# Kernel tuning notes

Hardware: AMD Instinct MI355X
Metric: run time of the kernel (lower is better)

The kernel has to match this reference:

```python
import jax, jax.numpy as jnp
import numpy as np

N_NODES = 100000
N_EDGES = 3200000
N_GRAPHS = 2048
MOL_DIM = 78
HID = 32
OUT = 128
N_LAYERS = 5
BN_EPS = 1e-5


def setup_inputs() -> dict:
    key = jax.random.key(0)
    ks = jax.random.split(key, 16)
    x = jax.random.normal(ks[0], (N_NODES, MOL_DIM), dtype=jnp.float32)
    edge_index = jax.random.randint(ks[1], (2, N_EDGES), 0, N_NODES, dtype=jnp.int32)
    batch = jnp.sort(jax.random.randint(ks[2], (N_NODES,), 0, N_GRAPHS, dtype=jnp.int32))
    def lin(k, fan_in, shape):
        b = 1.0 / np.sqrt(fan_in)
        return jax.random.uniform(k, shape, jnp.float32, -b, b)
    # layer 0 MLP (78 -> 32 -> 32)
    w1_0 = lin(ks[3], MOL_DIM, (MOL_DIM, HID))
    b1_0 = lin(ks[4], MOL_DIM, (HID,))
    w2_0 = lin(ks[5], HID, (HID, HID))
    b2_0 = lin(ks[6], HID, (HID,))
    # layers 1..4 MLPs (32 -> 32 -> 32), stacked
    w1 = lin(ks[7], HID, (N_LAYERS - 1, HID, HID))
    b1 = lin(ks[8], HID, (N_LAYERS - 1, HID))
    w2 = lin(ks[9], HID, (N_LAYERS - 1, HID, HID))
    b2 = lin(ks[10], HID, (N_LAYERS - 1, HID))
    # BatchNorm affine params per layer
    gamma = jnp.ones((N_LAYERS, HID), jnp.float32)
    beta = jnp.zeros((N_LAYERS, HID), jnp.float32)
    # final fc (32 -> 128)
    fc_w = lin(ks[11], HID, (HID, OUT))
    fc_b = lin(ks[12], HID, (OUT,))
    return {"x": x, "edge_index": edge_index, "batch": batch,
            "w1_0": w1_0, "b1_0": b1_0, "w2_0": w2_0, "b2_0": b2_0,
            "w1": w1, "b1": b1, "w2": w2, "b2": b2,
            "gamma": gamma, "beta": beta, "fc_w": fc_w, "fc_b": fc_b}


def _gin_layer(x, src, dst, W1, B1, W2, B2, g, bt):
    # GIN aggregation: (1+eps)*x + sum_{j in N(i)} x_j, eps = 0
    agg = x + jax.ops.segment_sum(x[src], dst, num_segments=N_NODES)
    h = jnp.maximum(agg @ W1 + B1, 0.0)   # Linear + ReLU
    h = h @ W2 + B2                        # Linear
    h = jnp.maximum(h, 0.0)                # outer act before BN
    mean = jnp.mean(h, axis=0)
    var = jnp.mean(jnp.square(h - mean), axis=0)  # biased (training BN)
    return (h - mean) * jax.lax.rsqrt(var + BN_EPS) * g + bt


def reference(x, edge_index, batch, w1_0, b1_0, w2_0, b2_0,
              w1, b1, w2, b2, gamma, beta, fc_w, fc_b):
    src, dst = edge_index[0], edge_index[1]
    h = _gin_layer(x, src, dst, w1_0, b1_0, w2_0, b2_0, gamma[0], beta[0])
    for i in range(N_LAYERS - 1):
        h = _gin_layer(h, src, dst, w1[i], b1[i], w2[i], b2[i],
                       gamma[i + 1], beta[i + 1])
    pooled = jax.ops.segment_sum(h, batch, num_segments=N_GRAPHS)  # [G, HID]
    out = jnp.maximum(pooled @ fc_w + fc_b, 0.0)  # dropout is identity in eval
    return out
```

## Files before the change

### kernel.cpp

```cpp
#include <hip/hip_runtime.h>
#include <hip/hip_fp16.h>

#define N_NODES 100000
#define N_EDGES 3200000
#define N_GRAPHS 2048
#define MOL 78
#define HID 32
#define OUTD 128
#define BN_EPS 1e-5f

#define NBUCK ((N_NODES + 255) / 256)
#define BCAP2 9216
#define EPB 4096
#define P1_BLOCKS ((N_EDGES + EPB - 1) / EPB)

#define NPH 4
#define CPL_BLOCKS (N_NODES / (8 * NPH))

#define NCOPY 64

__device__ inline unsigned int pkh2(float a, float b) {
    __half2 h = __halves2half2(__float2half_rn(a), __float2half_rn(b));
    return *(unsigned int*)&h;
}
__device__ inline float hlo(unsigned int v) {
    __half2 h = *(__half2*)&v;
    return __low2float(h);
}
__device__ inline float hhi(unsigned int v) {
    __half2 h = *(__half2*)&v;
    return __high2float(h);
}


__global__ __launch_bounds__(256) void part1_kernel(const int* __restrict__ src,
                                                    const int* __restrict__ dst,
                                                    int* __restrict__ gcur,
                                                    int* __restrict__ staging) {
    __shared__ int hist[NBUCK];
    __shared__ int lofs[NBUCK];
    __shared__ int lcur[NBUCK];
    __shared__ int gb[NBUCK];
    __shared__ int pk[EPB];
    __shared__ unsigned short bkt[EPB];
    __shared__ int sc[256];
    const int t = threadIdx.x;
    const int base = blockIdx.x * EPB;
    const int nedge = min(EPB, N_EDGES - base);

    for (int i = t; i < NBUCK; i += 256) hist[i] = 0;
    __syncthreads();
    for (int i = t; i < nedge; i += 256) atomicAdd(&hist[dst[base + i] >> 8], 1);
    __syncthreads();

    int a0 = (2 * t < NBUCK) ? hist[2 * t] : 0;
    int a1 = (2 * t + 1 < NBUCK) ? hist[2 * t + 1] : 0;
    int tot = a0 + a1;
    sc[t] = tot;
    __syncthreads();
    for (int off = 1; off < 256; off <<= 1) {
        int add = (t >= off) ? sc[t - off] : 0;
        __syncthreads();
        sc[t] += add;
        __syncthreads();
    }
    int excl = sc[t] - tot;
    if (2 * t < NBUCK) { lofs[2 * t] = excl; lcur[2 * t] = excl; }
    if (2 * t + 1 < NBUCK) { lofs[2 * t + 1] = excl + a0; lcur[2 * t + 1] = excl + a0; }
    __syncthreads();

    for (int i = t; i < nedge; i += 256) {
        int d = dst[base + i];
        int s = src[base + i];
        int b = d >> 8;
        int p = atomicAdd(&lcur[b], 1);
        pk[p] = (s << 8) | (d & 255);
        bkt[p] = (unsigned short)b;
    }
    __syncthreads();

    for (int b = t; b < NBUCK; b += 256) {
        int c = lcur[b] - lofs[b];
        gb[b] = c ? atomicAdd(&gcur[b], c) : 0;
    }
    __syncthreads();

    for (int i = t; i < nedge; i += 256) {
        int b = bkt[i];
        staging[(size_t)b * BCAP2 + gb[b] + (i - lofs[b])] = pk[i];
    }
}

__global__ void csrbase_kernel(const int* __restrict__ gcur, int* __restrict__ bbase,
                               int* __restrict__ row_start) {
    int t = threadIdx.x;
    int a0 = (2 * t < NBUCK) ? gcur[2 * t] : 0;
    int a1 = (2 * t + 1 < NBUCK) ? gcur[2 * t + 1] : 0;
    int tot = a0 + a1;
    __shared__ int sc[256];
    sc[t] = tot;
    __syncthreads();
    for (int off = 1; off < 256; off <<= 1) {
        int add = (t >= off) ? sc[t - off] : 0;
        __syncthreads();
        sc[t] += add;
        __syncthreads();
    }
    int excl = sc[t] - tot;
    if (2 * t < NBUCK) bbase[2 * t] = excl;
    if (2 * t + 1 < NBUCK) bbase[2 * t + 1] = excl + a0;
    if (t == 0) row_start[N_NODES] = N_EDGES;
}

__global__ __launch_bounds__(256) void part2_kernel(const int* __restrict__ gcur,
                                                    const int* __restrict__ bbase,
                                                    const int* __restrict__ staging,
                                                    int* __restrict__ row_start,
                                                    int* __restrict__ csr,
                                                    float* __restrict__ degf) {
    int b = blockIdx.x, t = threadIdx.x;
    __shared__ int ldeg[256];
    __shared__ int lex[256];
    __shared__ int sc[256];
    ldeg[t] = 0;
    __syncthreads();
    int cnt = gcur[b];
    int base = bbase[b];
    const int* sp = staging + (size_t)b * BCAP2;
    for (int i = t; i < cnt; i += 256) atomicAdd(&ldeg[sp[i] & 255], 1);
    __syncthreads();
    int v = ldeg[t];
    sc[t] = v;
    __syncthreads();
    for (int off = 1; off < 256; off <<= 1) {
        int add = (t >= off) ? sc[t - off] : 0;
        __syncthreads();
        sc[t] += add;
        __syncthreads();
    }
    int excl = sc[t] - v;
    int node = b * 256 + t;
    if (node < N_NODES) {
        row_start[node] = base + excl;
        degf[node] = 1.0f + (float)v;
    }
    lex[t] = base + excl;
    __syncthreads();
    for (int i = t; i < cnt; i += 256) {
        int pk = sp[i];
        int p = atomicAdd(&lex[pk & 255], 1);
        csr[p] = pk >> 8;
    }
}


__global__ void gcnt_kernel(const int* __restrict__ batch, int* __restrict__ cnt) {
    int g = blockIdx.x * blockDim.x + threadIdx.x;
    if (g >= N_GRAPHS) return;
    auto lb = [&](int key) {
        int lo = 0, hi = N_NODES;
        while (lo < hi) {
            int mid = (lo + hi) >> 1;
            if (batch[mid] < key) lo = mid + 1; else hi = mid;
        }
        return lo;
    };
    cnt[g] = lb(g + 1) - lb(g);
}


__global__ __launch_bounds__(256) void proj78_kernel(const float* __restrict__ in,
                                                     const float* __restrict__ W1,
                                                     unsigned int* __restrict__ y) {
    __shared__ float w1s[MOL * HID];
    for (int i = threadIdx.x; i < MOL * HID; i += 256) w1s[i] = W1[i];
    __syncthreads();
    const int node = blockIdx.x * 256 + threadIdx.x;
    if (node >= N_NODES) return;
    const float* row = in + (size_t)node * MOL;
    float acc[HID];
#pragma unroll
    for (int j = 0; j < HID; j++) acc[j] = 0.f;
    const float4* w1v = (const float4*)w1s;
    for (int k = 0; k < MOL; k++) {
        float xv = row[k];
#pragma unroll
        for (int q = 0; q < 8; q++) {
            float4 wv = w1v[k * 8 + q];
            acc[4 * q + 0] = fmaf(xv, wv.x, acc[4 * q + 0]);
            acc[4 * q + 1] = fmaf(xv, wv.y, acc[4 * q + 1]);
            acc[4 * q + 2] = fmaf(xv, wv.z, acc[4 * q + 2]);
            acc[4 * q + 3] = fmaf(xv, wv.w, acc[4 * q + 3]);
        }
    }
    uint4* o = (uint4*)(y + (size_t)node * 16);
#pragma unroll
    for (int g = 0; g < 4; g++) {
        uint4 u;
        u.x = pkh2(acc[8 * g + 0], acc[8 * g + 1]);
        u.y = pkh2(acc[8 * g + 2], acc[8 * g + 3]);
        u.z = pkh2(acc[8 * g + 4], acc[8 * g + 5]);
        u.w = pkh2(acc[8 * g + 6], acc[8 * g + 7]);
        o[g] = u;
    }
}


__global__ __launch_bounds__(256) void agg_kernel(const unsigned int* __restrict__ y,
                                                  const int* __restrict__ rs,
                                                  const int* __restrict__ csr,
                                                  float* __restrict__ agg) {
    int gt = blockIdx.x * blockDim.x + threadIdx.x;
    int node = gt >> 5;
    if (node >= N_NODES) return;
    int hl = threadIdx.x & 31;
    int s = hl >> 2;
    int q = hl & 3;
    const uint4* rows = (const uint4*)y;
    float acc[8];
#pragma unroll
    for (int i = 0; i < 8; i++) acc[i] = 0.f;
    if (s == 0) {
        uint4 u = rows[(size_t)node * 4 + q];
        acc[0] = hlo(u.x); acc[1] = hhi(u.x);
        acc[2] = hlo(u.y); acc[3] = hhi(u.y);
        acc[4] = hlo(u.z); acc[5] = hhi(u.z);
        acc[6] = hlo(u.w); acc[7] = hhi(u.w);
    }
    int e0 = rs[node], e1 = rs[node + 1];
    int k = e0 + s;
    for (; k + 8 < e1; k += 16) {
        uint4 a = rows[(size_t)csr[k] * 4 + q];
        uint4 b = rows[(size_t)csr[k + 8] * 4 + q];
        acc[0] += hlo(a.x) + hlo(b.x);
        acc[1] += hhi(a.x) + hhi(b.x);
        acc[2] += hlo(a.y) + hlo(b.y);
        acc[3] += hhi(a.y) + hhi(b.y);
        acc[4] += hlo(a.z) + hlo(b.z);
        acc[5] += hhi(a.z) + hhi(b.z);
        acc[6] += hlo(a.w) + hlo(b.w);
        acc[7] += hhi(a.w) + hhi(b.w);
    }
    if (k < e1) {
        uint4 a = rows[(size_t)csr[k] * 4 + q];
        acc[0] += hlo(a.x); acc[1] += hhi(a.x);
        acc[2] += hlo(a.y); acc[3] += hhi(a.y);
        acc[4] += hlo(a.z); acc[5] += hhi(a.z);
        acc[6] += hlo(a.w); acc[7] += hhi(a.w);
    }
#pragma unroll
    for (int m = 4; m <= 16; m <<= 1) {
#pragma unroll
        for (int i = 0; i < 8; i++) acc[i] += __shfl_xor(acc[i], m, 32);
    }
    if (s == 0) {
        float4* o = (float4*)(agg + (size_t)node * HID + q * 8);
        o[0] = make_float4(acc[0], acc[1], acc[2], acc[3]);
        o[1] = make_float4(acc[4], acc[5], acc[6], acc[7]);
    }
}


template <int MODE>
__global__ __launch_bounds__(256) void mlp_kernel(
    const float* __restrict__ aggb, const float* __restrict__ degf,
    const float* __restrict__ scsh_prev, const float* __restrict__ B1,
    const float* __restrict__ W1, const float* __restrict__ W2, const float* __restrict__ B2,
    __half* __restrict__ out, float* __restrict__ sums, const int* __restrict__ batch,
    float* __restrict__ pooledraw) {
    __shared__ float ldsu[8][NPH][HID];
    __shared__ float ldsv[8][NPH][HID];
    __shared__ float w2T[HID][HID + 1];
    __shared__ float w1T[HID][HID + 1];
    __shared__ float ssum[64];
    const int t = threadIdx.x;
    const int hw = t >> 5;
    const int c = t & 31;

    for (int idx = t; idx < HID * HID; idx += 256) {
        int k = idx >> 5, cc = idx & 31;
        w2T[cc][k] = W2[idx];
        if (MODE != 0) w1T[cc][k] = W1[idx];
    }
    if (t < 64) ssum[t] = 0.f;
    __syncthreads();

    const int n0 = (blockIdx.x * 8 + hw) * NPH;
    const float b2c = B2[c];
    float sl = 0.f, sq = 0.f;

    if (MODE == 0) {
        const float b1c = B1[c];
#pragma unroll
        for (int u = 0; u < NPH; u++)
            ldsu[hw][u][c] = fmaxf(aggb[(size_t)(n0 + u) * HID + c] + b1c, 0.f);
        float h[NPH];
#pragma unroll
        for (int u = 0; u < NPH; u++) h[u] = b2c;
#pragma unroll
        for (int qq = 0; qq < 8; qq++) {
            float wa = w2T[c][4 * qq + 0], wb = w2T[c][4 * qq + 1];
            float wc2 = w2T[c][4 * qq + 2], wd = w2T[c][4 * qq + 3];
#pragma unroll
            for (int u = 0; u < NPH; u++) {
                float4 vv = ((const float4*)&ldsu[hw][u][0])[qq];
                h[u] = fmaf(vv.x, wa, h[u]);
                h[u] = fmaf(vv.y, wb, h[u]);
                h[u] = fmaf(vv.z, wc2, h[u]);
                h[u] = fmaf(vv.w, wd, h[u]);
            }
        }
#pragma unroll
        for (int u = 0; u < NPH; u++) {
            float hv = fmaxf(h[u], 0.f);
            out[(size_t)(n0 + u) * 32 + c] = __float2half_rn(hv);
            sl += hv;
            sq += hv * hv;
        }
    } else {
        const float scv = scsh_prev[c], shv = scsh_prev[HID + c];
        const float b1c = B1[c];
#pragma unroll
        for (int u = 0; u < NPH; u++) {
            int n = n0 + u;
            ldsu[hw][u][c] = fmaf(aggb[(size_t)n * HID + c], scv, degf[n] * shv);
        }
        float tv[NPH];
#pragma unroll
        for (int u = 0; u < NPH; u++) tv[u] = b1c;
#pragma unroll
        for (int qq = 0; qq < 8; qq++) {
            float wa = w1T[c][4 * qq + 0], wb = w1T[c][4 * qq + 1];
            float wc1 = w1T[c][4 * qq + 2], wd = w1T[c][4 * qq + 3];
#pragma unroll
            for (int u = 0; u < NPH; u++) {
                float4 uu = ((const float4*)&ldsu[hw][u][0])[qq];
                tv[u] = fmaf(uu.x, wa, tv[u]);
                tv[u] = fmaf(uu.y, wb, tv[u]);
                tv[u] = fmaf(uu.z, wc1, tv[u]);
                tv[u] = fmaf(uu.w, wd, tv[u]);
            }
        }
#pragma unroll
        for (int u = 0; u < NPH; u++) ldsv[hw][u][c] = fmaxf(tv[u], 0.f);
        float h[NPH];
#pragma unroll
        for (int u = 0; u < NPH; u++) h[u] = b2c;
#pragma unroll
        for (int qq = 0; qq < 8; qq++) {
            float wa = w2T[c][4 * qq + 0], wb = w2T[c][4 * qq + 1];
            float wc2 = w2T[c][4 * qq + 2], wd = w2T[c][4 * qq + 3];
#pragma unroll
            for (int u = 0; u < NPH; u++) {
                float4 vv = ((const float4*)&ldsv[hw][u][0])[qq];
                h[u] = fmaf(vv.x, wa, h[u]);
                h[u] = fmaf(vv.y, wb, h[u]);
                h[u] = fmaf(vv.z, wc2, h[u]);
                h[u] = fmaf(vv.w, wd, h[u]);
            }
        }
#pragma unroll
        for (int u = 0; u < NPH; u++) {
            float hv = fmaxf(h[u], 0.f);
            if (MODE == 2) {
                atomicAdd(&pooledraw[batch[n0 + u] * HID + c], hv);
            } else {
                out[(size_t)(n0 + u) * 32 + c] = __float2half_rn(hv);
            }
            sl += hv;
            sq += hv * hv;
        }
    }

    atomicAdd(&ssum[c], sl);
    atomicAdd(&ssum[32 + c], sq);
    __syncthreads();
    if (t < 64) atomicAdd(&sums[(blockIdx.x & (NCOPY - 1)) * 64 + t], ssum[t]);
}


__global__ void bnfin_kernel(const float* __restrict__ sums, const float* __restrict__ g,
                             const float* __restrict__ bt, float* __restrict__ scsh) {
    __shared__ float red[64];
    int t = threadIdx.x;
    if (t < 64) {
        float acc = 0.f;
#pragma unroll 8
        for (int k = 0; k < NCOPY; k++) acc += sums[k * 64 + t];
        red[t] = acc;
    }
    __syncthreads();
    if (t < HID) {
        float m = red[t] * (1.0f / N_NODES);
        float var = red[HID + t] * (1.0f / N_NODES) - m * m;
        var = fmaxf(var, 0.f);
        float sc = g[t] * rsqrtf(var + BN_EPS);
        scsh[t] = sc;
        scsh[HID + t] = bt[t] - m * sc;
    }
}


__global__ void fc_kernel(const float* __restrict__ praw, const int* __restrict__ cnt,
                          const float* __restrict__ scsh4, const float* __restrict__ fcw,
                          const float* __restrict__ fcb, float* __restrict__ out) {
    __shared__ float w[HID * OUTD];
    __shared__ float aff[2 * HID];
    for (int i = threadIdx.x; i < HID * OUTD; i += 256) w[i] = fcw[i];
    if (threadIdx.x < 2 * HID) aff[threadIdx.x] = scsh4[threadIdx.x];
    __syncthreads();
    int idx = blockIdx.x * 256 + threadIdx.x;
    if (idx >= N_GRAPHS * OUTD) return;
    int g = idx >> 7;
    int o = idx & 127;
    float cg = (float)cnt[g];
    float acc = fcb[o];
#pragma unroll
    for (int k = 0; k < HID; k++) {
        float paff = fmaf(praw[g * HID + k], aff[k], cg * aff[HID + k]);
        acc = fmaf(paff, w[k * OUTD + o], acc);
    }
    out[idx] = fmaxf(acc, 0.f);
}


extern "C" void kernel_launch(void* const* d_in, const int* in_sizes, int n_in,
                              void* d_out, int out_size, void* d_ws, size_t ws_size,
                              hipStream_t stream) {
    const float* x = (const float*)d_in[0];
    const int* ei = (const int*)d_in[1];
    const int* batch = (const int*)d_in[2];
    const float* w1_0 = (const float*)d_in[3];
    const float* b1_0 = (const float*)d_in[4];
    const float* w2_0 = (const float*)d_in[5];
    const float* b2_0 = (const float*)d_in[6];
    const float* w1 = (const float*)d_in[7];
    const float* b1 = (const float*)d_in[8];
    const float* w2 = (const float*)d_in[9];
    const float* b2 = (const float*)d_in[10];
    const float* gamma = (const float*)d_in[11];
    const float* beta = (const float*)d_in[12];
    const float* fc_w = (const float*)d_in[13];
    const float* fc_b = (const float*)d_in[14];
    float* out = (float*)d_out;

    const int* e_src = ei;
    const int* e_dst = ei + N_EDGES;

    char* ws = (char*)d_ws;
    size_t off = 0;
    auto alloc = [&](size_t n) {
        void* p = ws + off;
        off += (n + 255) & ~(size_t)255;
        return p;
    };
    int* row_start = (int*)alloc((size_t)(N_NODES + 1) * 4);
    int* csr = (int*)alloc((size_t)N_EDGES * 4);
    int* bbase = (int*)alloc((size_t)NBUCK * 4);
    int* staging = (int*)alloc((size_t)NBUCK * BCAP2 * 4);
    unsigned int* hA = (unsigned int*)alloc((size_t)N_NODES * 16 * 4);
    unsigned int* hB = (unsigned int*)alloc((size_t)N_NODES * 16 * 4);
    float* aggb = (float*)alloc((size_t)N_NODES * HID * 4);
    float* degf = (float*)alloc((size_t)N_NODES * 4);
    float* scsh = (float*)alloc(5 * 2 * HID * 4);
    int* cnt = (int*)alloc((size_t)N_GRAPHS * 4);
    size_t zero_base = off;
    int* gcur = (int*)alloc((size_t)NBUCK * 4);
    float* bnsums = (float*)alloc((size_t)5 * NCOPY * 64 * 4);
    float* pooled = (float*)alloc((size_t)N_GRAPHS * HID * 4);
    size_t zero_len = off - zero_base;

    hipMemsetAsync(ws + zero_base, 0, zero_len, stream);

    part1_kernel<<<P1_BLOCKS, 256, 0, stream>>>(e_src, e_dst, gcur, staging);
    csrbase_kernel<<<1, 256, 0, stream>>>(gcur, bbase, row_start);
    part2_kernel<<<NBUCK, 256, 0, stream>>>(gcur, bbase, staging, row_start, csr, degf);
    gcnt_kernel<<<(N_GRAPHS + 255) / 256, 256, 0, stream>>>(batch, cnt);

    const int nodeBlocks = (N_NODES + 255) / 256;
    const int aggBlocks = (N_NODES * 32 + 255) / 256;

    proj78_kernel<<<nodeBlocks, 256, 0, stream>>>(x, w1_0, hA);
    agg_kernel<<<aggBlocks, 256, 0, stream>>>(hA, row_start, csr, aggb);
    mlp_kernel<0><<<CPL_BLOCKS, 256, 0, stream>>>(aggb, nullptr, nullptr, b1_0, nullptr, w2_0,
                                                  b2_0, (__half*)hB, bnsums, nullptr, nullptr);
    bnfin_kernel<<<1, 64, 0, stream>>>(bnsums, gamma, beta, scsh);

    unsigned int* cur = hB;
    unsigned int* nxt = hA;
    for (int l = 1; l < 5; l++) {
        int i = l - 1;
        agg_kernel<<<aggBlocks, 256, 0, stream>>>(cur, row_start, csr, aggb);
        if (l < 4) {
            mlp_kernel<1><<<CPL_BLOCKS, 256, 0, stream>>>(
                aggb, degf, scsh + (l - 1) * 2 * HID, b1 + (size_t)i * HID,
                w1 + (size_t)i * HID * HID, w2 + (size_t)i * HID * HID, b2 + (size_t)i * HID,
                (__half*)nxt, bnsums + (size_t)l * NCOPY * 64, nullptr, nullptr);
            unsigned int* tmp = cur; cur = nxt; nxt = tmp;
        } else {
            mlp_kernel<2><<<CPL_BLOCKS, 256, 0, stream>>>(
                aggb, degf, scsh + (l - 1) * 2 * HID, b1 + (size_t)i * HID,
                w1 + (size_t)i * HID * HID, w2 + (size_t)i * HID * HID, b2 + (size_t)i * HID,
                nullptr, bnsums + (size_t)l * NCOPY * 64, batch, pooled);
        }
        bnfin_kernel<<<1, 64, 0, stream>>>(bnsums + (size_t)l * NCOPY * 64, gamma + l * HID,
                                           beta + l * HID, scsh + l * 2 * HID);
    }

    fc_kernel<<<(N_GRAPHS * OUTD + 255) / 256, 256, 0, stream>>>(
        pooled, cnt, scsh + 4 * 2 * HID, fc_w, fc_b, out);
}
```

Before: 431.8 us.

## Fold BatchNorm affine into next layer W1 and keep MLP weights in registers

The previous layer's BN scale is folded into a pre-transposed W1 (and its shift into a degree-weighted bias b1s) inside bnfin, so mlp no longer applies the affine per element. A new prep kernel pre-transposes W2 for all layers, letting mlp load its weight rows straight into registers instead of staging them in LDS, and aggregated inputs are read directly from global memory rather than through an LDS tile. This removes per-block weight staging and a shared-memory pass, at the cost of more registers per thread (launch bounds now request 4 blocks) and redundant per-lane global reads of aggb.

Result: slower. 509.1 us (+17.9%).

```diff
diff --git a/kernel.cpp b/kernel.cpp
--- a/kernel.cpp
+++ b/kernel.cpp
@@ -169,6 +169,18 @@
 }
 
 
+__global__ void wprep_kernel(const float* __restrict__ w2_0, const float* __restrict__ w2,
+                             float* __restrict__ w2Tg) {
+    int idx = blockIdx.x * blockDim.x + threadIdx.x;
+    if (idx >= 5 * HID * HID) return;
+    int l = idx >> 10;
+    int r = idx & 1023;
+    int k = r >> 5, c = r & 31;
+    const float* srcm = (l == 0) ? w2_0 : (w2 + (size_t)(l - 1) * HID * HID);
+    w2Tg[(size_t)l * HID * HID + c * HID + k] = srcm[k * HID + c];
+}
+
+
 __global__ __launch_bounds__(256) void proj78_kernel(const float* __restrict__ in,
                                                      const float* __restrict__ W1,
                                                      unsigned int* __restrict__ y) {
@@ -262,26 +274,17 @@
 
 
 template <int MODE>
-__global__ __launch_bounds__(256) void mlp_kernel(
+__global__ __launch_bounds__(256, 4) void mlp_kernel(
     const float* __restrict__ aggb, const float* __restrict__ degf,
-    const float* __restrict__ scsh_prev, const float* __restrict__ B1,
-    const float* __restrict__ W1, const float* __restrict__ W2, const float* __restrict__ B2,
-    __half* __restrict__ out, float* __restrict__ sums, const int* __restrict__ batch,
-    float* __restrict__ pooledraw) {
-    __shared__ float ldsu[8][NPH][HID];
+    const float* __restrict__ B1, const float* __restrict__ b1s,
+    const float* __restrict__ w1Tg, const float* __restrict__ w2Tg,
+    const float* __restrict__ B2, __half* __restrict__ out, float* __restrict__ sums,
+    const int* __restrict__ batch, float* __restrict__ pooledraw) {
     __shared__ float ldsv[8][NPH][HID];
-    __shared__ float w2T[HID][HID + 1];
-    __shared__ float w1T[HID][HID + 1];
     __shared__ float ssum[64];
     const int t = threadIdx.x;
     const int hw = t >> 5;
     const int c = t & 31;
-
-    for (int idx = t; idx < HID * HID; idx += 256) {
-        int k = idx >> 5, cc = idx & 31;
-        w2T[cc][k] = W2[idx];
-        if (MODE != 0) w1T[cc][k] = W1[idx];
-    }
     if (t < 64) ssum[t] = 0.f;
     __syncthreads();
 
@@ -289,25 +292,32 @@
     const float b2c = B2[c];
     float sl = 0.f, sq = 0.f;
 
+    float4 w2r[8];
+    const float4* w2p = (const float4*)(w2Tg + (size_t)c * HID);
+#pragma unroll
+    for (int qq = 0; qq < 8; qq++) w2r[qq] = w2p[qq];
+
     if (MODE == 0) {
-        const float b1c = B1[c];
-#pragma unroll
-        for (int u = 0; u < NPH; u++)
-            ldsu[hw][u][c] = fmaxf(aggb[(size_t)(n0 + u) * HID + c] + b1c, 0.f);
+        float4 b1v[8];
+        const float4* b1p = (const float4*)B1;
+#pragma unroll
+        for (int qq = 0; qq < 8; qq++) b1v[qq] = b1p[qq];
         float h[NPH];
 #pragma unroll
         for (int u = 0; u < NPH; u++) h[u] = b2c;
 #pragma unroll
         for (int qq = 0; qq < 8; qq++) {
-            float wa = w2T[c][4 * qq + 0], wb = w2T[c][4 * qq + 1];
-            float wc2 = w2T[c][4 * qq + 2], wd = w2T[c][4 * qq + 3];
 #pragma unroll
             for (int u = 0; u < NPH; u++) {
-                float4 vv = ((const float4*)&ldsu[hw][u][0])[qq];
-                h[u] = fmaf(vv.x, wa, h[u]);
-                h[u] = fmaf(vv.y, wb, h[u]);
-                h[u] = fmaf(vv.z, wc2, h[u]);
-                h[u] = fmaf(vv.w, wd, h[u]);
+                float4 a = ((const float4*)(aggb + (size_t)(n0 + u) * HID))[qq];
+                float vx = fmaxf(a.x + b1v[qq].x, 0.f);
+                float vy = fmaxf(a.y + b1v[qq].y, 0.f);
+                float vz = fmaxf(a.z + b1v[qq].z, 0.f);
+                float vw = fmaxf(a.w + b1v[qq].w, 0.f);
+                h[u] = fmaf(vx, w2r[qq].x, h[u]);
+                h[u] = fmaf(vy, w2r[qq].y, h[u]);
+                h[u] = fmaf(vz, w2r[qq].z, h[u]);
+                h[u] = fmaf(vw, w2r[qq].w, h[u]);
             }
         }
 #pragma unroll
@@ -318,27 +328,24 @@
             sq += hv * hv;
         }
     } else {
-        const float scv = scsh_prev[c], shv = scsh_prev[HID + c];
+        float4 w1r[8];
+        const float4* w1p = (const float4*)(w1Tg + (size_t)c * HID);
+#pragma unroll
+        for (int qq = 0; qq < 8; qq++) w1r[qq] = w1p[qq];
         const float b1c = B1[c];
-#pragma unroll
-        for (int u = 0; u < NPH; u++) {
-            int n = n0 + u;
-            ldsu[hw][u][c] = fmaf(aggb[(size_t)n * HID + c], scv, degf[n] * shv);
-        }
+        const float b1sc = b1s[c];
         float tv[NPH];
 #pragma unroll
-        for (int u = 0; u < NPH; u++) tv[u] = b1c;
+        for (int u = 0; u < NPH; u++) tv[u] = fmaf(degf[n0 + u], b1sc, b1c);
 #pragma unroll
         for (int qq = 0; qq < 8; qq++) {
-            float wa = w1T[c][4 * qq + 0], wb = w1T[c][4 * qq + 1];
-            float wc1 = w1T[c][4 * qq + 2], wd = w1T[c][4 * qq + 3];
 #pragma unroll
             for (int u = 0; u < NPH; u++) {
-                float4 uu = ((const float4*)&ldsu[hw][u][0])[qq];
-                tv[u] = fmaf(uu.x, wa, tv[u]);
-                tv[u] = fmaf(uu.y, wb, tv[u]);
-                tv[u] = fmaf(uu.z, wc1, tv[u]);
-                tv[u] = fmaf(uu.w, wd, tv[u]);
+                float4 a = ((const float4*)(aggb + (size_t)(n0 + u) * HID))[qq];
+                tv[u] = fmaf(a.x, w1r[qq].x, tv[u]);
+                tv[u] = fmaf(a.y, w1r[qq].y, tv[u]);
+                tv[u] = fmaf(a.z, w1r[qq].z, tv[u]);
+                tv[u] = fmaf(a.w, w1r[qq].w, tv[u]);
             }
         }
 #pragma unroll
@@ -348,15 +355,13 @@
         for (int u = 0; u < NPH; u++) h[u] = b2c;
 #pragma unroll
         for (int qq = 0; qq < 8; qq++) {
-            float wa = w2T[c][4 * qq + 0], wb = w2T[c][4 * qq + 1];
-            float wc2 = w2T[c][4 * qq + 2], wd = w2T[c][4 * qq + 3];
 #pragma unroll
             for (int u = 0; u < NPH; u++) {
                 float4 vv = ((const float4*)&ldsv[hw][u][0])[qq];
-                h[u] = fmaf(vv.x, wa, h[u]);
-                h[u] = fmaf(vv.y, wb, h[u]);
-                h[u] = fmaf(vv.z, wc2, h[u]);
-                h[u] = fmaf(vv.w, wd, h[u]);
+                h[u] = fmaf(vv.x, w2r[qq].x, h[u]);
+                h[u] = fmaf(vv.y, w2r[qq].y, h[u]);
+                h[u] = fmaf(vv.z, w2r[qq].z, h[u]);
+                h[u] = fmaf(vv.w, w2r[qq].w, h[u]);
             }
         }
 #pragma unroll
@@ -380,8 +385,11 @@
 
 
 __global__ void bnfin_kernel(const float* __restrict__ sums, const float* __restrict__ g,
-                             const float* __restrict__ bt, float* __restrict__ scsh) {
+                             const float* __restrict__ bt, float* __restrict__ scsh,
+                             const float* __restrict__ W1src, float* __restrict__ w1Tg,
+                             float* __restrict__ b1s) {
     __shared__ float red[64];
+    __shared__ float s_sc[HID], s_sh[HID];
     int t = threadIdx.x;
     if (t < 64) {
         float acc = 0.f;
@@ -395,8 +403,23 @@
         float var = red[HID + t] * (1.0f / N_NODES) - m * m;
         var = fmaxf(var, 0.f);
         float sc = g[t] * rsqrtf(var + BN_EPS);
+        float sh = bt[t] - m * sc;
         scsh[t] = sc;
-        scsh[HID + t] = bt[t] - m * sc;
+        scsh[HID + t] = sh;
+        s_sc[t] = sc;
+        s_sh[t] = sh;
+    }
+    __syncthreads();
+    if (W1src) {
+        for (int idx = t; idx < HID * HID; idx += 256) {
+            int k = idx >> 5, c = idx & 31;
+            w1Tg[c * HID + k] = s_sc[k] * W1src[idx];
+        }
+        if (t < HID) {
+            float b = 0.f;
+            for (int k = 0; k < HID; k++) b = fmaf(s_sh[k], W1src[k * HID + t], b);
+            b1s[t] = b;
+        }
     }
 }
 
@@ -463,6 +486,9 @@
     float* aggb = (float*)alloc((size_t)N_NODES * HID * 4);
     float* degf = (float*)alloc((size_t)N_NODES * 4);
     float* scsh = (float*)alloc(5 * 2 * HID * 4);
+    float* w2Tg = (float*)alloc(5 * HID * HID * 4);
+    float* w1Tg = (float*)alloc(4 * HID * HID * 4);
+    float* b1s = (float*)alloc(4 * HID * 4);
     int* cnt = (int*)alloc((size_t)N_GRAPHS * 4);
     size_t zero_base = off;
     int* gcur = (int*)alloc((size_t)NBUCK * 4);
@@ -476,15 +502,16 @@
     csrbase_kernel<<<1, 256, 0, stream>>>(gcur, bbase, row_start);
     part2_kernel<<<NBUCK, 256, 0, stream>>>(gcur, bbase, staging, row_start, csr, degf);
     gcnt_kernel<<<(N_GRAPHS + 255) / 256, 256, 0, stream>>>(batch, cnt);
+    wprep_kernel<<<(5 * HID * HID + 255) / 256, 256, 0, stream>>>(w2_0, w2, w2Tg);
 
     const int nodeBlocks = (N_NODES + 255) / 256;
     const int aggBlocks = (N_NODES * 32 + 255) / 256;
 
     proj78_kernel<<<nodeBlocks, 256, 0, stream>>>(x, w1_0, hA);
     agg_kernel<<<aggBlocks, 256, 0, stream>>>(hA, row_start, csr, aggb);
-    mlp_kernel<0><<<CPL_BLOCKS, 256, 0, stream>>>(aggb, nullptr, nullptr, b1_0, nullptr, w2_0,
+    mlp_kernel<0><<<CPL_BLOCKS, 256, 0, stream>>>(aggb, nullptr, b1_0, nullptr, nullptr, w2Tg,
                                                   b2_0, (__half*)hB, bnsums, nullptr, nullptr);
-    bnfin_kernel<<<1, 64, 0, stream>>>(bnsums, gamma, beta, scsh);
+    bnfin_kernel<<<1, 256, 0, stream>>>(bnsums, gamma, beta, scsh, w1, w1Tg, b1s);
 
     unsigned int* cur = hB;
     unsigned int* nxt = hA;
@@ -493,18 +520,22 @@
         agg_kernel<<<aggBlocks, 256, 0, stream>>>(cur, row_start, csr, aggb);
         if (l < 4) {
             mlp_kernel<1><<<CPL_BLOCKS, 256, 0, stream>>>(
-                aggb, degf, scsh + (l - 1) * 2 * HID, b1 + (size_t)i * HID,
-                w1 + (size_t)i * HID * HID, w2 + (size_t)i * HID * HID, b2 + (size_t)i * HID,
-                (__half*)nxt, bnsums + (size_t)l * NCOPY * 64, nullptr, nullptr);
+                aggb, degf, b1 + (size_t)i * HID, b1s + (size_t)i * HID,
+                w1Tg + (size_t)i * HID * HID, w2Tg + (size_t)l * HID * HID,
+                b2 + (size_t)i * HID, (__half*)nxt, bnsums + (size_t)l * NCOPY * 64, nullptr,
+                nullptr);
             unsigned int* tmp = cur; cur = nxt; nxt = tmp;
         } else {
             mlp_kernel<2><<<CPL_BLOCKS, 256, 0, stream>>>(
-                aggb, degf, scsh + (l - 1) * 2 * HID, b1 + (size_t)i * HID,
-                w1 + (size_t)i * HID * HID, w2 + (size_t)i * HID * HID, b2 + (size_t)i * HID,
-                nullptr, bnsums + (size_t)l * NCOPY * 64, batch, pooled);
-        }
-        bnfin_kernel<<<1, 64, 0, stream>>>(bnsums + (size_t)l * NCOPY * 64, gamma + l * HID,
-                                           beta + l * HID, scsh + l * 2 * HID);
+                aggb, degf, b1 + (size_t)i * HID, b1s + (size_t)i * HID,
+                w1Tg + (size_t)i * HID * HID, w2Tg + (size_t)l * HID * HID,
+                b2 + (size_t)i * HID, nullptr, bnsums + (size_t)l * NCOPY * 64, batch, pooled);
+        }
+        const float* w1next = (l < 4) ? (w1 + (size_t)l * HID * HID) : nullptr;
+        bnfin_kernel<<<1, 256, 0, stream>>>(bnsums + (size_t)l * NCOPY * 64, gamma + l * HID,
+                                            beta + l * HID, scsh + l * 2 * HID, w1next,
+                                            w1Tg + (size_t)l * HID * HID,
+                                            b1s + (size_t)l * HID);
     }
 
     fc_kernel<<<(N_GRAPHS * OUTD + 255) / 256, 256, 0, stream>>>(
```
